# Performance work log

Hardware: AMD Instinct MI355X
Metric: run time of the kernel (lower is better)

## Reference

```python
import jax, jax.numpy as jnp
import numpy as np

B, S, F, H = 16, 2048, 1024, 16
D = F // H
EPS = 1e-5


def setup_inputs() -> dict:
    key = jax.random.key(0)
    ks = jax.random.split(key, 10)
    scale = 1.0 / np.sqrt(F)
    return {
        "x": jax.random.normal(ks[0], (B, S, F), jnp.float32),
        "Wq": jax.random.normal(ks[1], (F, F), jnp.float32) * scale,
        "bq": jnp.zeros((F,), jnp.float32),
        "Wk": jax.random.normal(ks[2], (F, F), jnp.float32) * scale,
        "bk": jnp.zeros((F,), jnp.float32),
        "Wv": jax.random.normal(ks[3], (F, F), jnp.float32) * scale,
        "bv": jnp.zeros((F,), jnp.float32),
        "Wo": jax.random.normal(ks[4], (F, F), jnp.float32) * scale,
        "bo": jnp.zeros((F,), jnp.float32),
        "gamma": jnp.ones((F,), jnp.float32),
        "beta": jnp.zeros((F,), jnp.float32),
    }


def reference(x, Wq, bq, Wk, bk, Wv, bv, Wo, bo, gamma, beta):
    # x: (B, S, F). Dropout is identity in eval mode.
    b, s, f = x.shape
    q = (x @ Wq + bq).reshape(b, s, H, D)
    k = (x @ Wk + bk).reshape(b, s, H, D)
    v = (x @ Wv + bv).reshape(b, s, H, D)
    # Faithful to source: the einsum (applied to permuted tensors) contracts
    # across HEADS at each sequence position -> scores (B, S, H, H).
    energy = jnp.einsum('bshd,bsgd->bshg', q, k) / (D ** 0.5)
    attn = jax.nn.softmax(energy, axis=-1)  # softmax over key-head axis
    out = jnp.einsum('bshg,bsgd->bshd', attn, v).reshape(b, s, f)
    out = out @ Wo + bo
    # LayerNorm over last dim (eps=1e-5, affine)
    mu = jnp.mean(out, axis=-1, keepdims=True)
    var = jnp.mean((out - mu) ** 2, axis=-1, keepdims=True)
    return (out - mu) * jax.lax.rsqrt(var + EPS) * gamma + beta
```

## Files before the change

kernel.cpp:

```cpp
#include <hip/hip_runtime.h>
#include <hip/hip_bf16.h>
#include <stdint.h>

#define MM   32768
#define FFD  1024
#define NQKV 3072

typedef __bf16 bf16x8 __attribute__((ext_vector_type(8)));
typedef float  f32x4  __attribute__((ext_vector_type(4)));

__device__ __forceinline__ unsigned short f2bf_bits(float f){
  __hip_bfloat16 h = __float2bfloat16(f);
  unsigned short u;
  __builtin_memcpy(&u, &h, 2);
  return u;
}

__device__ __forceinline__ void gld16(const void* g, void* l){
  const unsigned int* gu = (const unsigned int*)g;
  unsigned int* lu = (unsigned int*)l;
  __builtin_amdgcn_global_load_lds(
      (const __attribute__((address_space(1))) unsigned int*)gu,
      (__attribute__((address_space(3))) unsigned int*)lu,
      16, 0, 0);
}

#define BARRIER() do { asm volatile("" ::: "memory"); \
                       __builtin_amdgcn_s_barrier();  \
                       asm volatile("" ::: "memory"); } while(0)

__global__ __launch_bounds__(256) void k_convert_bf16(const float* __restrict__ in,
                                                      unsigned short* __restrict__ out,
                                                      int n4){
  int i = blockIdx.x * 256 + threadIdx.x;
  if (i >= n4) return;
  float4 v = ((const float4*)in)[i];
  ushort4 r;
  r.x = f2bf_bits(v.x); r.y = f2bf_bits(v.y);
  r.z = f2bf_bits(v.z); r.w = f2bf_bits(v.w);
  ((ushort4*)out)[i] = r;
}

__global__ __launch_bounds__(256) void k_transpose_bf16(const float* __restrict__ in,
                                                        unsigned short* __restrict__ out,
                                                        int rows, int cols){
  __shared__ float tile[32][33];
  int bc = blockIdx.x * 32, br = blockIdx.y * 32;
  int tx = threadIdx.x, ty = threadIdx.y;
  #pragma unroll
  for (int j = 0; j < 32; j += 8)
    tile[ty + j][tx] = in[(size_t)(br + ty + j) * cols + bc + tx];
  __syncthreads();
  #pragma unroll
  for (int j = 0; j < 32; j += 8)
    out[(size_t)(bc + ty + j) * rows + br + tx] = f2bf_bits(tile[tx][ty + j]);
}

template <bool BF16OUT>
__global__ __launch_bounds__(512, 2) void k_gemm_bt(
    const unsigned short* __restrict__ A,
    const unsigned short* __restrict__ Bt,
    const float* __restrict__ b0, const float* __restrict__ b1, const float* __restrict__ b2,
    void* __restrict__ Cout, int M, int N, int K)
{
  __shared__ alignas(16) char smem[131072];

  const int tid  = threadIdx.x;
  const int lane = tid & 63;
  const int wave = tid >> 6;
  const int wr = wave >> 2, wc = wave & 3;
  const int quad = lane >> 4, lrow = lane & 15;
  const int sa = ((lrow >> 1) & 3) << 4;

  const int nwgx = gridDim.x;
  int nwg = nwgx * gridDim.y;
  int bid = blockIdx.y * nwgx + blockIdx.x;
  int cpx = nwg >> 3;
  int nid = (bid & 7) * cpx + (bid >> 3);
  int by = nid / nwgx;
  int bx = nid - by * nwgx;

  const long rowBase = (long)by * 256;
  const long colBase = (long)bx * 256;

  f32x4 acc[8][4];
  #pragma unroll
  for (int i = 0; i < 8; i++)
    #pragma unroll
    for (int j = 0; j < 4; j++)
      acc[i][j] = (f32x4){0.f, 0.f, 0.f, 0.f};

  const int swz8 = 8 * ((tid & 3) ^ ((tid >> 3) & 3));
  const unsigned short* gA = A  + (rowBase + (tid >> 2)) * (long)K + swz8;
  const unsigned short* gB = Bt + (colBase + (tid >> 2)) * (long)K + swz8;
  const long hstep = 128L * K;

  const int nk = K >> 5;

  #pragma unroll
  for (int tt = 0; tt < 3; ++tt){
    char* nb = smem + tt * 32768;
    gld16(gA + tt * 32,         nb +         tid * 16);
    gld16(gA + tt * 32 + hstep, nb +  8192 + tid * 16);
    gld16(gB + tt * 32,         nb + 16384 + tid * 16);
    gld16(gB + tt * 32 + hstep, nb + 24576 + tid * 16);
  }

  for (int t = 0; t < nk; ++t){
    if (t <= nk - 3)      asm volatile("s_waitcnt vmcnt(8)" ::: "memory");
    else if (t == nk - 2) asm volatile("s_waitcnt vmcnt(4)" ::: "memory");
    else                  asm volatile("s_waitcnt vmcnt(0)" ::: "memory");
    BARRIER();

    char* buf = smem + (t & 3) * 32768;
    if (t < nk - 3){
      char* nb = smem + ((t + 3) & 3) * 32768;
      const unsigned short* sA = gA + (long)(t + 3) * 32;
      const unsigned short* sB = gB + (long)(t + 3) * 32;
      gld16(sA,         nb +         tid * 16);
      gld16(sA + hstep, nb +  8192 + tid * 16);
      gld16(sB,         nb + 16384 + tid * 16);
      gld16(sB + hstep, nb + 24576 + tid * 16);
    }

    bf16x8 bfr[4];
    const char* bb = buf + 16384 + wc * 4096 + lrow * 64 + ((quad * 16) ^ sa);
    #pragma unroll
    for (int n = 0; n < 4; ++n)
      bfr[n] = *(const bf16x8*)(bb + n * 1024);

    #pragma unroll
    for (int p = 0; p < 2; ++p){
      bf16x8 af[4];
      const char* ab = buf + wr * 8192 + p * 4096 + lrow * 64 + ((quad * 16) ^ sa);
      #pragma unroll
      for (int f = 0; f < 4; ++f)
        af[f] = *(const bf16x8*)(ab + f * 1024);
      __builtin_amdgcn_s_setprio(1);
      #pragma unroll
      for (int f = 0; f < 4; ++f)
        #pragma unroll
        for (int n = 0; n < 4; ++n)
          acc[p * 4 + f][n] =
              __builtin_amdgcn_mfma_f32_16x16x32_bf16(af[f], bfr[n], acc[p * 4 + f][n], 0, 0, 0);
      __builtin_amdgcn_s_setprio(0);
    }
  }

  if constexpr (BF16OUT){
    BARRIER();
    #pragma unroll
    for (int n = 0; n < 4; ++n){
      int lcol = wc * 64 + n * 16 + lrow;
      long col = colBase + lcol;
      const float* bp = (col < 1024) ? b0 : ((col < 2048) ? b1 : b2);
      float bias = bp[col & 1023];
      #pragma unroll
      for (int m = 0; m < 8; ++m){
        int row0 = wr * 128 + (m >> 2) * 64 + (m & 3) * 16 + quad * 4;
        int sw = ((row0 >> 2) & 3) << 5;
        #pragma unroll
        for (int r = 0; r < 4; ++r){
          float v = acc[m][n][r] + bias;
          int byte = (row0 + r) * 512 + ((lcol * 2) ^ sw);
          *(unsigned short*)(smem + byte) = f2bf_bits(v);
        }
      }
    }
    asm volatile("s_waitcnt lgkmcnt(0)" ::: "memory");
    BARRIER();
    unsigned short* Cb = (unsigned short*)Cout;
    #pragma unroll
    for (int i = 0; i < 16; ++i){
      int c = i * 512 + tid;
      int row = c >> 5, cidx = c & 31;
      int rb = (cidx ^ (((row >> 2) & 3) << 1)) * 16;
      uint4 u = *(const uint4*)(smem + row * 512 + rb);
      *(uint4*)(Cb + (rowBase + row) * (long)N + colBase + cidx * 8) = u;
    }
  } else {
    #pragma unroll
    for (int n = 0; n < 4; ++n){
      long col = colBase + wc * 64 + n * 16 + lrow;
      const float* bp = (col < 1024) ? b0 : ((col < 2048) ? b1 : b2);
      float bias = bp[col & 1023];
      #pragma unroll
      for (int m = 0; m < 8; ++m){
        long row0 = rowBase + wr * 128 + (m >> 2) * 64 + (m & 3) * 16 + quad * 4;
        #pragma unroll
        for (int r = 0; r < 4; ++r){
          float v = acc[m][n][r] + bias;
          ((float*)Cout)[(row0 + r) * (long)N + col] = v;
        }
      }
    }
  }
}

__global__ __launch_bounds__(256) void k_attention(const unsigned short* __restrict__ qkv,
                                                   unsigned short* __restrict__ aout){
  const int lane = threadIdx.x & 63;
  const int wave = threadIdx.x >> 6;
  const int pos  = blockIdx.x * 4 + wave;
  const int quad = lane >> 4, lidx = lane & 15;

  const unsigned short* src = qkv + (size_t)pos * 3072;

  f32x4 s = (f32x4){0.f, 0.f, 0.f, 0.f};
  #pragma unroll
  for (int kk = 0; kk < 2; ++kk){
    bf16x8 aK = *(const bf16x8*)(src + 1024 + lidx * 64 + kk * 32 + quad * 8);
    bf16x8 bQ = *(const bf16x8*)(src +        lidx * 64 + kk * 32 + quad * 8);
    s = __builtin_amdgcn_mfma_f32_16x16x32_bf16(aK, bQ, s, 0, 0, 0);
  }

  float v0 = s[0] * 0.125f, v1 = s[1] * 0.125f;
  float v2 = s[2] * 0.125f, v3 = s[3] * 0.125f;
  float m = fmaxf(fmaxf(v0, v1), fmaxf(v2, v3));
  m = fmaxf(m, __shfl_xor(m, 16));
  m = fmaxf(m, __shfl_xor(m, 32));
  float e0 = __expf(v0 - m), e1 = __expf(v1 - m);
  float e2 = __expf(v2 - m), e3 = __expf(v3 - m);
  float sum = e0 + e1 + e2 + e3;
  sum += __shfl_xor(sum, 16);
  sum += __shfl_xor(sum, 32);
  float inv = 1.0f / sum;
  unsigned P01 = (unsigned)f2bf_bits(e0 * inv) | ((unsigned)f2bf_bits(e1 * inv) << 16);
  unsigned P23 = (unsigned)f2bf_bits(e2 * inv) | ((unsigned)f2bf_bits(e3 * inv) << 16);

  int sA = ((quad * 32) + lidx) & 63;
  int sB = (sA + 16) & 63;
  unsigned w0 = (unsigned)__shfl((int)P01, sA);
  unsigned w1 = (unsigned)__shfl((int)P23, sA);
  unsigned w2 = (unsigned)__shfl((int)P01, sB);
  unsigned w3 = (unsigned)__shfl((int)P23, sB);
  if (quad >= 2){ w0 = 0u; w1 = 0u; w2 = 0u; w3 = 0u; }
  union { unsigned u[4]; bf16x8 v; } bp;
  bp.u[0] = w0; bp.u[1] = w1; bp.u[2] = w2; bp.u[3] = w3;

  const unsigned short* Vp = src + 2048;
  unsigned short* dst = aout + (size_t)pos * 1024;
  #pragma unroll
  for (int n4 = 0; n4 < 4; ++n4){
    union { unsigned short us[8]; bf16x8 v; } av;
    #pragma unroll
    for (int j = 0; j < 8; ++j){
      unsigned short rv = Vp[((quad * 8 + j) & 15) * 64 + n4 * 16 + lidx];
      av.us[j] = (quad < 2) ? rv : (unsigned short)0;
    }
    f32x4 o = __builtin_amdgcn_mfma_f32_16x16x32_bf16(
        av.v, bp.v, (f32x4){0.f, 0.f, 0.f, 0.f}, 0, 0, 0);
    unsigned lo = (unsigned)f2bf_bits(o[0]) | ((unsigned)f2bf_bits(o[1]) << 16);
    unsigned hi = (unsigned)f2bf_bits(o[2]) | ((unsigned)f2bf_bits(o[3]) << 16);
    uint2 st; st.x = lo; st.y = hi;
    *(uint2*)(dst + lidx * 64 + n4 * 16 + quad * 4) = st;
  }
}

__global__ __launch_bounds__(256) void k_ln(float* __restrict__ out,
                                            const float* __restrict__ gamma,
                                            const float* __restrict__ beta){
  __shared__ float red[8];
  int tid = threadIdx.x;
  float4* rowp = (float4*)(out + (size_t)blockIdx.x * 1024);
  float4 v = rowp[tid];
  float s  = v.x + v.y + v.z + v.w;
  float ss = v.x * v.x + v.y * v.y + v.z * v.z + v.w * v.w;
  #pragma unroll
  for (int off = 32; off > 0; off >>= 1){
    s  += __shfl_down(s, off);
    ss += __shfl_down(ss, off);
  }
  if ((tid & 63) == 0){ red[tid >> 6] = s; red[4 + (tid >> 6)] = ss; }
  __syncthreads();
  float S  = red[0] + red[1] + red[2] + red[3];
  float SS = red[4] + red[5] + red[6] + red[7];
  float mean = S * (1.0f / 1024.0f);
  float var  = SS * (1.0f / 1024.0f) - mean * mean;
  float rstd = rsqrtf(var + 1e-5f);
  float4 g = ((const float4*)gamma)[tid];
  float4 b = ((const float4*)beta)[tid];
  v.x = (v.x - mean) * rstd * g.x + b.x;
  v.y = (v.y - mean) * rstd * g.y + b.y;
  v.z = (v.z - mean) * rstd * g.z + b.z;
  v.w = (v.w - mean) * rstd * g.w + b.w;
  rowp[tid] = v;
}

extern "C" void kernel_launch(void* const* d_in, const int* in_sizes, int n_in,
                              void* d_out, int out_size, void* d_ws, size_t ws_size,
                              hipStream_t stream){
  const float* x     = (const float*)d_in[0];
  const float* Wq    = (const float*)d_in[1];
  const float* bq    = (const float*)d_in[2];
  const float* Wk    = (const float*)d_in[3];
  const float* bk    = (const float*)d_in[4];
  const float* Wv    = (const float*)d_in[5];
  const float* bv    = (const float*)d_in[6];
  const float* Wo    = (const float*)d_in[7];
  const float* bo    = (const float*)d_in[8];
  const float* gamma = (const float*)d_in[9];
  const float* beta  = (const float*)d_in[10];
  float* out = (float*)d_out;

  char* ws = (char*)d_ws;
  unsigned short* Wqkv_t = (unsigned short*)ws;
  unsigned short* Wo_t   = (unsigned short*)(ws + 6291456);
  unsigned short* xb     = (unsigned short*)(ws + 8388608);
  unsigned short* qkv    = (unsigned short*)(ws + 75497472);
  unsigned short* aout   = xb;

  k_convert_bf16<<<32768, 256, 0, stream>>>(x, xb, (MM * FFD) / 4);

  dim3 tb(32, 8), tg(32, 32);
  k_transpose_bf16<<<tg, tb, 0, stream>>>(Wq, Wqkv_t,                1024, 1024);
  k_transpose_bf16<<<tg, tb, 0, stream>>>(Wk, Wqkv_t + 1024 * 1024,  1024, 1024);
  k_transpose_bf16<<<tg, tb, 0, stream>>>(Wv, Wqkv_t + 2048 * 1024,  1024, 1024);
  k_transpose_bf16<<<tg, tb, 0, stream>>>(Wo, Wo_t,                  1024, 1024);

  k_gemm_bt<true><<<dim3(NQKV / 256, MM / 256), 512, 0, stream>>>(
      xb, Wqkv_t, bq, bk, bv, qkv, MM, NQKV, FFD);

  k_attention<<<MM / 4, 256, 0, stream>>>(qkv, aout);

  k_gemm_bt<false><<<dim3(FFD / 256, MM / 256), 512, 0, stream>>>(
      aout, Wo_t, bo, bo, bo, out, MM, FFD, FFD);

  k_ln<<<MM, 256, 0, stream>>>(out, gamma, beta);
}
```

Measured before the change: 643.9 us.

## Fuse LayerNorm statistics into output GEMM epilogue and store bf16 intermediate

The output projection GEMM now computes per-row sum and sum-of-squares in its epilogue, reduces them with shuffles and atomics into a stats buffer, and writes its result as bf16 through the swizzled LDS path. A light LN kernel then reads the bf16 rows plus the precomputed stats and writes fp32 output. This removes the fp32 scattered store from the GEMM and the separate reduction pass. The four weight transposes are also merged into one launch. Risks are atomic contention, bf16 rounding of the pre-norm values, and a stats buffer that overlays the no-longer-needed Wqkv_t workspace after the QKV GEMM.

```diff
diff --git a/kernel.cpp b/kernel.cpp
--- a/kernel.cpp
+++ b/kernel.cpp
@@ -14,6 +14,13 @@
   unsigned short u;
   __builtin_memcpy(&u, &h, 2);
   return u;
+}
+
+__device__ __forceinline__ float bf2f(unsigned short u){
+  unsigned v = ((unsigned)u) << 16;
+  float f;
+  __builtin_memcpy(&f, &v, 4);
+  return f;
 }
 
 __device__ __forceinline__ void gld16(const void* g, void* l){
@@ -41,27 +48,38 @@
   ((ushort4*)out)[i] = r;
 }
 
-__global__ __launch_bounds__(256) void k_transpose_bf16(const float* __restrict__ in,
-                                                        unsigned short* __restrict__ out,
-                                                        int rows, int cols){
+__global__ __launch_bounds__(256) void k_transpose4(const float* __restrict__ Wq,
+                                                    const float* __restrict__ Wk,
+                                                    const float* __restrict__ Wv,
+                                                    const float* __restrict__ Wo,
+                                                    unsigned short* __restrict__ Wqkv_t,
+                                                    unsigned short* __restrict__ Wo_t){
   __shared__ float tile[32][33];
+  const float* in;
+  unsigned short* out;
+  switch (blockIdx.z){
+    case 0:  in = Wq; out = Wqkv_t;               break;
+    case 1:  in = Wk; out = Wqkv_t + 1024 * 1024; break;
+    case 2:  in = Wv; out = Wqkv_t + 2048 * 1024; break;
+    default: in = Wo; out = Wo_t;                 break;
+  }
   int bc = blockIdx.x * 32, br = blockIdx.y * 32;
-  int tx = threadIdx.x, ty = threadIdx.y;
+  int tx = threadIdx.x & 31, ty = threadIdx.x >> 5;
   #pragma unroll
   for (int j = 0; j < 32; j += 8)
-    tile[ty + j][tx] = in[(size_t)(br + ty + j) * cols + bc + tx];
+    tile[ty + j][tx] = in[(size_t)(br + ty + j) * 1024 + bc + tx];
   __syncthreads();
   #pragma unroll
   for (int j = 0; j < 32; j += 8)
-    out[(size_t)(bc + ty + j) * rows + br + tx] = f2bf_bits(tile[tx][ty + j]);
-}
-
-template <bool BF16OUT>
+    out[(size_t)(bc + ty + j) * 1024 + br + tx] = f2bf_bits(tile[tx][ty + j]);
+}
+
+template <bool STATS>
 __global__ __launch_bounds__(512, 2) void k_gemm_bt(
     const unsigned short* __restrict__ A,
     const unsigned short* __restrict__ Bt,
     const float* __restrict__ b0, const float* __restrict__ b1, const float* __restrict__ b2,
-    void* __restrict__ Cout, int M, int N, int K)
+    unsigned short* __restrict__ Cout, float* __restrict__ stats, int M, int N, int K)
 {
   __shared__ alignas(16) char smem[131072];
 
@@ -147,53 +165,63 @@
     }
   }
 
-  if constexpr (BF16OUT){
-    BARRIER();
-    #pragma unroll
-    for (int n = 0; n < 4; ++n){
-      int lcol = wc * 64 + n * 16 + lrow;
-      long col = colBase + lcol;
-      const float* bp = (col < 1024) ? b0 : ((col < 2048) ? b1 : b2);
-      float bias = bp[col & 1023];
+  float biasv[4];
+  #pragma unroll
+  for (int n = 0; n < 4; ++n){
+    long col = colBase + wc * 64 + n * 16 + lrow;
+    const float* bp = (col < 1024) ? b0 : ((col < 2048) ? b1 : b2);
+    biasv[n] = bp[col & 1023];
+  }
+
+  if constexpr (STATS){
+    #pragma unroll
+    for (int m = 0; m < 8; ++m){
       #pragma unroll
-      for (int m = 0; m < 8; ++m){
-        int row0 = wr * 128 + (m >> 2) * 64 + (m & 3) * 16 + quad * 4;
-        int sw = ((row0 >> 2) & 3) << 5;
+      for (int r = 0; r < 4; ++r){
+        float p = 0.f, q = 0.f;
         #pragma unroll
-        for (int r = 0; r < 4; ++r){
-          float v = acc[m][n][r] + bias;
-          int byte = (row0 + r) * 512 + ((lcol * 2) ^ sw);
-          *(unsigned short*)(smem + byte) = f2bf_bits(v);
+        for (int n = 0; n < 4; ++n){
+          float v = acc[m][n][r] + biasv[n];
+          p += v; q += v * v;
+        }
+        p += __shfl_xor(p, 1);  q += __shfl_xor(q, 1);
+        p += __shfl_xor(p, 2);  q += __shfl_xor(q, 2);
+        p += __shfl_xor(p, 4);  q += __shfl_xor(q, 4);
+        p += __shfl_xor(p, 8);  q += __shfl_xor(q, 8);
+        if (lrow == 0){
+          long row = rowBase + wr * 128 + (m >> 2) * 64 + (m & 3) * 16 + quad * 4 + r;
+          atomicAdd(&stats[row * 2],     p);
+          atomicAdd(&stats[row * 2 + 1], q);
         }
       }
     }
-    asm volatile("s_waitcnt lgkmcnt(0)" ::: "memory");
-    BARRIER();
-    unsigned short* Cb = (unsigned short*)Cout;
-    #pragma unroll
-    for (int i = 0; i < 16; ++i){
-      int c = i * 512 + tid;
-      int row = c >> 5, cidx = c & 31;
-      int rb = (cidx ^ (((row >> 2) & 3) << 1)) * 16;
-      uint4 u = *(const uint4*)(smem + row * 512 + rb);
-      *(uint4*)(Cb + (rowBase + row) * (long)N + colBase + cidx * 8) = u;
-    }
-  } else {
-    #pragma unroll
-    for (int n = 0; n < 4; ++n){
-      long col = colBase + wc * 64 + n * 16 + lrow;
-      const float* bp = (col < 1024) ? b0 : ((col < 2048) ? b1 : b2);
-      float bias = bp[col & 1023];
+  }
+
+  BARRIER();
+  #pragma unroll
+  for (int n = 0; n < 4; ++n){
+    int lcol = wc * 64 + n * 16 + lrow;
+    #pragma unroll
+    for (int m = 0; m < 8; ++m){
+      int row0 = wr * 128 + (m >> 2) * 64 + (m & 3) * 16 + quad * 4;
+      int sw = ((row0 >> 2) & 3) << 5;
       #pragma unroll
-      for (int m = 0; m < 8; ++m){
-        long row0 = rowBase + wr * 128 + (m >> 2) * 64 + (m & 3) * 16 + quad * 4;
-        #pragma unroll
-        for (int r = 0; r < 4; ++r){
-          float v = acc[m][n][r] + bias;
-          ((float*)Cout)[(row0 + r) * (long)N + col] = v;
-        }
+      for (int r = 0; r < 4; ++r){
+        float v = acc[m][n][r] + biasv[n];
+        int byte = (row0 + r) * 512 + ((lcol * 2) ^ sw);
+        *(unsigned short*)(smem + byte) = f2bf_bits(v);
       }
     }
+  }
+  asm volatile("s_waitcnt lgkmcnt(0)" ::: "memory");
+  BARRIER();
+  #pragma unroll
+  for (int i = 0; i < 16; ++i){
+    int c = i * 512 + tid;
+    int row = c >> 5, cidx = c & 31;
+    int rb = (cidx ^ (((row >> 2) & 3) << 1)) * 16;
+    uint4 u = *(const uint4*)(smem + row * 512 + rb);
+    *(uint4*)(Cout + (rowBase + row) * (long)N + colBase + cidx * 8) = u;
   }
 }
 
@@ -257,34 +285,26 @@
   }
 }
 
-__global__ __launch_bounds__(256) void k_ln(float* __restrict__ out,
-                                            const float* __restrict__ gamma,
-                                            const float* __restrict__ beta){
-  __shared__ float red[8];
-  int tid = threadIdx.x;
-  float4* rowp = (float4*)(out + (size_t)blockIdx.x * 1024);
-  float4 v = rowp[tid];
-  float s  = v.x + v.y + v.z + v.w;
-  float ss = v.x * v.x + v.y * v.y + v.z * v.z + v.w * v.w;
-  #pragma unroll
-  for (int off = 32; off > 0; off >>= 1){
-    s  += __shfl_down(s, off);
-    ss += __shfl_down(ss, off);
-  }
-  if ((tid & 63) == 0){ red[tid >> 6] = s; red[4 + (tid >> 6)] = ss; }
-  __syncthreads();
-  float S  = red[0] + red[1] + red[2] + red[3];
-  float SS = red[4] + red[5] + red[6] + red[7];
-  float mean = S * (1.0f / 1024.0f);
-  float var  = SS * (1.0f / 1024.0f) - mean * mean;
+__global__ __launch_bounds__(256) void k_ln_stats(const unsigned short* __restrict__ ob,
+                                                  const float* __restrict__ stats,
+                                                  const float* __restrict__ gamma,
+                                                  const float* __restrict__ beta,
+                                                  float* __restrict__ out){
+  int row = blockIdx.x, tid = threadIdx.x;
+  float s  = stats[row * 2];
+  float ss = stats[row * 2 + 1];
+  float mean = s * (1.0f / 1024.0f);
+  float var  = ss * (1.0f / 1024.0f) - mean * mean;
   float rstd = rsqrtf(var + 1e-5f);
+  ushort4 u = ((const ushort4*)(ob + (size_t)row * 1024))[tid];
   float4 g = ((const float4*)gamma)[tid];
   float4 b = ((const float4*)beta)[tid];
-  v.x = (v.x - mean) * rstd * g.x + b.x;
-  v.y = (v.y - mean) * rstd * g.y + b.y;
-  v.z = (v.z - mean) * rstd * g.z + b.z;
-  v.w = (v.w - mean) * rstd * g.w + b.w;
-  rowp[tid] = v;
+  float4 v;
+  v.x = (bf2f(u.x) - mean) * rstd * g.x + b.x;
+  v.y = (bf2f(u.y) - mean) * rstd * g.y + b.y;
+  v.z = (bf2f(u.z) - mean) * rstd * g.z + b.z;
+  v.w = (bf2f(u.w) - mean) * rstd * g.w + b.w;
+  ((float4*)(out + (size_t)row * 1024))[tid] = v;
 }
 
 extern "C" void kernel_launch(void* const* d_in, const int* in_sizes, int n_in,
@@ -309,22 +329,22 @@
   unsigned short* xb     = (unsigned short*)(ws + 8388608);
   unsigned short* qkv    = (unsigned short*)(ws + 75497472);
   unsigned short* aout   = xb;
+  float*          stats  = (float*)ws;
+  unsigned short* obf    = qkv;
 
   k_convert_bf16<<<32768, 256, 0, stream>>>(x, xb, (MM * FFD) / 4);
 
-  dim3 tb(32, 8), tg(32, 32);
-  k_transpose_bf16<<<tg, tb, 0, stream>>>(Wq, Wqkv_t,                1024, 1024);
-  k_transpose_bf16<<<tg, tb, 0, stream>>>(Wk, Wqkv_t + 1024 * 1024,  1024, 1024);
-  k_transpose_bf16<<<tg, tb, 0, stream>>>(Wv, Wqkv_t + 2048 * 1024,  1024, 1024);
-  k_transpose_bf16<<<tg, tb, 0, stream>>>(Wo, Wo_t,                  1024, 1024);
-
-  k_gemm_bt<true><<<dim3(NQKV / 256, MM / 256), 512, 0, stream>>>(
-      xb, Wqkv_t, bq, bk, bv, qkv, MM, NQKV, FFD);
+  k_transpose4<<<dim3(32, 32, 4), 256, 0, stream>>>(Wq, Wk, Wv, Wo, Wqkv_t, Wo_t);
+
+  k_gemm_bt<false><<<dim3(NQKV / 256, MM / 256), 512, 0, stream>>>(
+      xb, Wqkv_t, bq, bk, bv, qkv, nullptr, MM, NQKV, FFD);
+
+  hipMemsetAsync(stats, 0, MM * 2 * sizeof(float), stream);
 
   k_attention<<<MM / 4, 256, 0, stream>>>(qkv, aout);
 
-  k_gemm_bt<false><<<dim3(FFD / 256, MM / 256), 512, 0, stream>>>(
-      aout, Wo_t, bo, bo, bo, out, MM, FFD, FFD);
-
-  k_ln<<<MM, 256, 0, stream>>>(out, gamma, beta);
-}
+  k_gemm_bt<true><<<dim3(FFD / 256, MM / 256), 512, 0, stream>>>(
+      aout, Wo_t, bo, bo, bo, obf, stats, MM, FFD, FFD);
+
+  k_ln_stats<<<MM, 256, 0, stream>>>(obf, stats, gamma, beta, out);
+}
```

Result: slower. 673.7 us (+4.6%).
